# Performance work log

Measured on AMD Instinct MI355X. Metric: run time of the kernel, lower is better.

## Reference

```python
import jax, jax.numpy as jnp
import numpy as np
import math

B, S, D = 4, 2048, 1024
NUM_HEADS = 16
HEAD_DIM = D // NUM_HEADS


def setup_inputs() -> dict:
    key = jax.random.key(0)
    ks = jax.random.split(key, 6)
    scale = 1.0 / math.sqrt(D)
    batch = jax.random.normal(ks[0], (B, S, D), dtype=jnp.float32)
    w_query = jax.random.normal(ks[1], (D, D), dtype=jnp.float32) * scale
    w_key = jax.random.normal(ks[2], (D, D), dtype=jnp.float32) * scale
    w_value = jax.random.normal(ks[3], (D, D), dtype=jnp.float32) * scale
    out_w = jax.random.normal(ks[4], (D, D), dtype=jnp.float32) * scale
    out_b = jax.random.normal(ks[5], (D,), dtype=jnp.float32) * 0.01
    return {"batch": batch, "w_query": w_query, "w_key": w_key,
            "w_value": w_value, "out_w": out_w, "out_b": out_b}


def reference(batch, w_query, w_key, w_value, out_w, out_b):
    b, s, _ = batch.shape
    # QKV projections (Linear with no bias): x @ W^T, here weights stored as [D,D] applied as x@W
    q = (batch @ w_query).reshape(b, s, NUM_HEADS, HEAD_DIM)
    k = (batch @ w_key).reshape(b, s, NUM_HEADS, HEAD_DIM)
    v = (batch @ w_value).reshape(b, s, NUM_HEADS, HEAD_DIM)
    # scores: [b, h, s, s]
    scores = jnp.einsum('bqhd,bkhd->bhqk', q, k)
    causal = jnp.tril(jnp.ones((s, s), dtype=bool))
    scores = jnp.where(causal, scores, -jnp.inf)
    # original divides by sqrt(head_dim) AFTER masking (-inf stays -inf)
    weights = jax.nn.softmax(scores / math.sqrt(HEAD_DIM), axis=-1)
    # dropout_percent = 0 -> identity
    out = jnp.einsum('bhqk,bkhd->bqhd', weights, v).reshape(b, s, D)
    return out @ out_w + out_b
```

## Files before the change

kernel.cpp:

```cpp
#include <hip/hip_runtime.h>
#include <hip/hip_bf16.h>

#define S_LEN 2048
#define D_DIM 1024
#define NHEAD 16
#define HDIM  64
#define BATCH 4
#define MROWS (BATCH*S_LEN)
#define QKV_LD 3072

typedef short bf16x8 __attribute__((ext_vector_type(8)));
typedef float f32x4  __attribute__((ext_vector_type(4)));
typedef float f32x16 __attribute__((ext_vector_type(16)));
typedef unsigned short u16;

#if __has_builtin(__builtin_amdgcn_exp2f)
#define EXP2(x) __builtin_amdgcn_exp2f(x)
#else
#define EXP2(x) __expf((x) * 0.6931471805599453f)
#endif

__device__ inline u16 f2bf(float f) {
  union { float f; unsigned u; } v; v.f = f;
  unsigned r = v.u + 0x7fff + ((v.u >> 16) & 1);
  return (u16)(r >> 16);
}

__device__ inline unsigned cvtpk(float lo, float hi_) {
  unsigned d;
  asm("v_cvt_pk_bf16_f32 %0, %1, %2" : "=v"(d) : "v"(lo), "v"(hi_));
  return d;
}

__device__ inline void perm32swap(unsigned& a, unsigned& b) {
  asm volatile("v_permlane32_swap_b32 %0, %1" : "+v"(a), "+v"(b));
}

__device__ inline void gload_lds16(const void* g, void* l) {
  __builtin_amdgcn_global_load_lds(
      (const __attribute__((address_space(1))) void*)g,
      (__attribute__((address_space(3))) void*)l, 16, 0, 0);
}

__global__ void cvt_x_kernel(const float* __restrict__ x, u16* __restrict__ xb, int n4) {
  int i = blockIdx.x * 256 + threadIdx.x;
  if (i >= n4) return;
  float4 v = reinterpret_cast<const float4*>(x)[i];
  ushort4 o;
  o.x = f2bf(v.x); o.y = f2bf(v.y); o.z = f2bf(v.z); o.w = f2bf(v.w);
  reinterpret_cast<ushort4*>(xb)[i] = o;
}

__global__ void transpose_w_kernel(const float* __restrict__ w, u16* __restrict__ wt) {
  __shared__ float t[32][33];
  int tx = threadIdx.x, ty = threadIdx.y;
  int n0 = blockIdx.x * 32, k0 = blockIdx.y * 32;
#pragma unroll
  for (int j = 0; j < 32; j += 8)
    t[ty + j][tx] = w[(size_t)(k0 + ty + j) * D_DIM + n0 + tx];
  __syncthreads();
#pragma unroll
  for (int j = 0; j < 32; j += 8)
    wt[(size_t)(n0 + ty + j) * D_DIM + k0 + tx] = f2bf(t[tx][ty + j]);
}

__global__ __launch_bounds__(256) void pack_k_kernel(const u16* __restrict__ QKV,
                                                     u16* __restrict__ KP) {
  int tid = threadIdx.x;
  int j = blockIdx.x, bh = blockIdx.y;
  int s = tid >> 6, lane = tid & 63;
  int lq = lane & 31, hi = lane >> 5;
  int b = bh >> 4, h = bh & 15;
  const u16* src = QKV + (size_t)(b * S_LEN + j * 32 + lq) * QKV_LD
                   + 1024 + h * HDIM + s * 16 + hi * 8;
  bf16x8 v = *(const bf16x8*)src;
  *(bf16x8*)(KP + ((size_t)(bh * 64 + j) * 4 + s) * 512 + lane * 8) = v;
}

__global__ __launch_bounds__(256) void pack_v_kernel(const u16* __restrict__ QKV,
                                                     u16* __restrict__ VP) {
  int tid = threadIdx.x;
  int j = blockIdx.x, bh = blockIdx.y;
  int c = tid >> 6, lane = tid & 63;
  int lq = lane & 31, hi = lane >> 5;
  int b = bh >> 4, h = bh & 15;
  int d = (c >> 1) * 32 + lq;
  int s0 = j * 32 + (c & 1) * 16 + hi * 8;
  const u16* src = QKV + (size_t)(b * S_LEN + s0) * QKV_LD + 2048 + h * HDIM + d;
  u16 tmp[8];
#pragma unroll
  for (int e = 0; e < 8; ++e) tmp[e] = src[(size_t)e * QKV_LD];
  *(bf16x8*)(VP + ((size_t)(bh * 64 + j) * 4 + c) * 512 + lane * 8) = *(bf16x8*)tmp;
}

template <int EPI>
__global__ __launch_bounds__(256) void gemm_bt_kernel(
    const u16* __restrict__ A, const u16* __restrict__ Bt,
    void* __restrict__ Cv, const float* __restrict__ bias, int ldc) {
  __shared__ u16 lA[128 * 32];
  __shared__ u16 lB[128 * 32];
  const int tid = threadIdx.x, wid = tid >> 6, lane = tid & 63;
  const int bm = blockIdx.y, bn = blockIdx.x;
  const int fr = lane & 15, fq = lane >> 4;
  const int r0 = wid * 32;
  const int srow = lane >> 2, scol = (lane & 3) * 8;
  const u16* gA = A + (size_t)(bm * 128 + r0 + srow) * 1024 + scol;
  const u16* gB = Bt + (size_t)(bn * 128 + r0 + srow) * 1024 + scol;
  u16* lA0 = &lA[r0 * 32];
  u16* lB0 = &lB[r0 * 32];

  f32x4 acc[4][4] = {};
  const int wm = (wid >> 1) * 64, wn = (wid & 1) * 64;

  for (int k0 = 0; k0 < 1024; k0 += 32) {
    gload_lds16(gA + k0,             lA0);
    gload_lds16(gA + k0 + 16 * 1024, lA0 + 16 * 32);
    gload_lds16(gB + k0,             lB0);
    gload_lds16(gB + k0 + 16 * 1024, lB0 + 16 * 32);
    __syncthreads();
    bf16x8 fa[4], fb[4];
#pragma unroll
    for (int i = 0; i < 4; i++) {
      fa[i] = *(const bf16x8*)&lA[(wm + i * 16 + fr) * 32 + fq * 8];
      fb[i] = *(const bf16x8*)&lB[(wn + i * 16 + fr) * 32 + fq * 8];
    }
#pragma unroll
    for (int i = 0; i < 4; i++)
#pragma unroll
      for (int j = 0; j < 4; j++)
        acc[i][j] = __builtin_amdgcn_mfma_f32_16x16x32_bf16(fa[i], fb[j], acc[i][j], 0, 0, 0);
    __syncthreads();
  }

#pragma unroll
  for (int i = 0; i < 4; i++)
#pragma unroll
    for (int j = 0; j < 4; j++)
#pragma unroll
      for (int r = 0; r < 4; r++) {
        int row = bm * 128 + wm + i * 16 + fq * 4 + r;
        int col = bn * 128 + wn + j * 16 + fr;
        if (EPI == 0) {
          ((u16*)Cv)[(size_t)row * ldc + col] = f2bf(acc[i][j][r]);
        } else {
          ((float*)Cv)[(size_t)row * ldc + col] = acc[i][j][r] + bias[col];
        }
      }
}

__global__ __launch_bounds__(256) void attn_kernel(
    const u16* __restrict__ QKV, const u16* __restrict__ KP,
    const u16* __restrict__ VP, u16* __restrict__ O) {
  const int tid = threadIdx.x, wid = tid >> 6, lane = tid & 63;
  const int lq = lane & 31, hi = lane >> 5;
  int f = blockIdx.x;
  int xcd = f & 7, kk = f >> 3;
  int bh = xcd * 8 + (kk & 7);
  int qblk = 15 - (kk >> 3);
  int b = bh >> 4, h = bh & 15;
  int q0 = qblk * 128 + wid * 32;
  int q = q0 + lq;

  const u16* Qrow = QKV + (size_t)(b * S_LEN + q) * QKV_LD + h * HDIM;
  bf16x8 qf[4];
#pragma unroll
  for (int s = 0; s < 4; s++)
    qf[s] = *(const bf16x8*)(Qrow + s * 16 + hi * 8);

  const bf16x8* KPt = (const bf16x8*)KP + (size_t)bh * 64 * 4 * 64;
  const bf16x8* VPt = (const bf16x8*)VP + (size_t)bh * 64 * 4 * 64;

  f32x16 acc0 = {}, acc1 = {};
  float m = -3.0e38f, l = 0.f;
  const int nt = qblk * 4 + wid + 1;

  for (int t = 0; t < nt; ++t) {
    const int j0 = t * 32;
    const size_t fb = (size_t)t * 4 * 64 + lane;
    bf16x8 kf0 = KPt[fb], kf1 = KPt[fb + 64], kf2 = KPt[fb + 128], kf3 = KPt[fb + 192];
    bf16x8 vf00 = VPt[fb], vf01 = VPt[fb + 64], vf10 = VPt[fb + 128], vf11 = VPt[fb + 192];

    f32x16 sa = {};
    __builtin_amdgcn_s_setprio(1);
    sa = __builtin_amdgcn_mfma_f32_32x32x16_bf16(kf0, qf[0], sa, 0, 0, 0);
    sa = __builtin_amdgcn_mfma_f32_32x32x16_bf16(kf1, qf[1], sa, 0, 0, 0);
    sa = __builtin_amdgcn_mfma_f32_32x32x16_bf16(kf2, qf[2], sa, 0, 0, 0);
    sa = __builtin_amdgcn_mfma_f32_32x32x16_bf16(kf3, qf[3], sa, 0, 0, 0);
    __builtin_amdgcn_s_setprio(0);

    float p[16];
#pragma unroll
    for (int r = 0; r < 16; ++r) p[r] = sa[r] * 0.1803368801f;

    if (t == nt - 1) {
#pragma unroll
      for (int r = 0; r < 16; ++r) {
        int kidx = j0 + (r & 3) + 8 * (r >> 2) + 4 * hi;
        if (kidx > q) p[r] = -3.0e38f;
      }
    }

    float x8[8], x4[4], x2[2];
#pragma unroll
    for (int i = 0; i < 8; ++i) x8[i] = fmaxf(p[2 * i], p[2 * i + 1]);
#pragma unroll
    for (int i = 0; i < 4; ++i) x4[i] = fmaxf(x8[2 * i], x8[2 * i + 1]);
    x2[0] = fmaxf(x4[0], x4[1]); x2[1] = fmaxf(x4[2], x4[3]);
    float pm = fmaxf(x2[0], x2[1]);
    pm = fmaxf(pm, __shfl_xor(pm, 32));

    if (__any(pm > m + 11.5f)) {
      float mn = fmaxf(m, pm);
      float sc = EXP2(m - mn);
      l *= sc;
#pragma unroll
      for (int r = 0; r < 16; ++r) { acc0[r] *= sc; acc1[r] *= sc; }
      m = mn;
    }

    float rs = 0.f;
#pragma unroll
    for (int r = 0; r < 16; ++r) { p[r] = EXP2(p[r] - m); rs += p[r]; }
    rs += __shfl_xor(rs, 32);
    l += rs;

    unsigned c0 = cvtpk(p[0],  p[1]),  c1 = cvtpk(p[2],  p[3]);
    unsigned c2 = cvtpk(p[4],  p[5]),  c3 = cvtpk(p[6],  p[7]);
    unsigned c4 = cvtpk(p[8],  p[9]),  c5 = cvtpk(p[10], p[11]);
    unsigned c6 = cvtpk(p[12], p[13]), c7 = cvtpk(p[14], p[15]);
    perm32swap(c0, c2); perm32swap(c1, c3);
    perm32swap(c4, c6); perm32swap(c5, c7);
    union U4 { unsigned u[4]; bf16x8 v; } F0, F1;
    F0.u[0] = c0; F0.u[1] = c1; F0.u[2] = c2; F0.u[3] = c3;
    F1.u[0] = c4; F1.u[1] = c5; F1.u[2] = c6; F1.u[3] = c7;

    __builtin_amdgcn_s_setprio(1);
    acc0 = __builtin_amdgcn_mfma_f32_32x32x16_bf16(vf00, F0.v, acc0, 0, 0, 0);
    acc0 = __builtin_amdgcn_mfma_f32_32x32x16_bf16(vf01, F1.v, acc0, 0, 0, 0);
    acc1 = __builtin_amdgcn_mfma_f32_32x32x16_bf16(vf10, F0.v, acc1, 0, 0, 0);
    acc1 = __builtin_amdgcn_mfma_f32_32x32x16_bf16(vf11, F1.v, acc1, 0, 0, 0);
    __builtin_amdgcn_s_setprio(0);
  }

  float inv = 1.f / l;
  u16* Orow = O + (size_t)(b * S_LEN + q) * D_DIM + h * HDIM;
#pragma unroll
  for (int g = 0; g < 4; ++g) {
    ushort4 o4;
    o4.x = f2bf(acc0[g * 4 + 0] * inv);
    o4.y = f2bf(acc0[g * 4 + 1] * inv);
    o4.z = f2bf(acc0[g * 4 + 2] * inv);
    o4.w = f2bf(acc0[g * 4 + 3] * inv);
    *(ushort4*)(Orow + 8 * g + 4 * hi) = o4;
  }
#pragma unroll
  for (int g = 0; g < 4; ++g) {
    ushort4 o4;
    o4.x = f2bf(acc1[g * 4 + 0] * inv);
    o4.y = f2bf(acc1[g * 4 + 1] * inv);
    o4.z = f2bf(acc1[g * 4 + 2] * inv);
    o4.w = f2bf(acc1[g * 4 + 3] * inv);
    *(ushort4*)(Orow + 32 + 8 * g + 4 * hi) = o4;
  }
}

extern "C" void kernel_launch(void* const* d_in, const int* in_sizes, int n_in,
                              void* d_out, int out_size, void* d_ws, size_t ws_size,
                              hipStream_t stream) {
  const float* x  = (const float*)d_in[0];
  const float* wq = (const float*)d_in[1];
  const float* wk = (const float*)d_in[2];
  const float* wv = (const float*)d_in[3];
  const float* wo = (const float*)d_in[4];
  const float* ob = (const float*)d_in[5];
  float* out = (float*)d_out;

  char* ws = (char*)d_ws;
  u16* Xb    = (u16*)(ws);
  u16* Ab    = (u16*)(ws);
  u16* QKV   = (u16*)(ws + (size_t)16 * 1024 * 1024);
  u16* KPb   = (u16*)(ws + (size_t)64 * 1024 * 1024);
  u16* VPb   = (u16*)(ws + (size_t)80 * 1024 * 1024);
  u16* WqkvT = (u16*)(ws + (size_t)96 * 1024 * 1024);
  u16* WoT   = (u16*)(ws + (size_t)102 * 1024 * 1024);

  cvt_x_kernel<<<(MROWS * D_DIM / 4) / 256, 256, 0, stream>>>(x, Xb, MROWS * D_DIM / 4);

  dim3 tb(32, 8);
  transpose_w_kernel<<<dim3(32, 32), tb, 0, stream>>>(wq, WqkvT);
  transpose_w_kernel<<<dim3(32, 32), tb, 0, stream>>>(wk, WqkvT + 1024 * 1024);
  transpose_w_kernel<<<dim3(32, 32), tb, 0, stream>>>(wv, WqkvT + 2 * 1024 * 1024);
  transpose_w_kernel<<<dim3(32, 32), tb, 0, stream>>>(wo, WoT);

  gemm_bt_kernel<0><<<dim3(QKV_LD / 128, MROWS / 128), 256, 0, stream>>>(
      Xb, WqkvT, QKV, nullptr, QKV_LD);

  pack_k_kernel<<<dim3(64, 64), 256, 0, stream>>>(QKV, KPb);
  pack_v_kernel<<<dim3(64, 64), 256, 0, stream>>>(QKV, VPb);

  attn_kernel<<<dim3(1024), 256, 0, stream>>>(QKV, KPb, VPb, Ab);

  gemm_bt_kernel<1><<<dim3(D_DIM / 128, MROWS / 128), 256, 0, stream>>>(
      Ab, WoT, out, ob, D_DIM);
}
```

Measured before the change: 187.0 us.

## Replace GEMM with 256x256 eight-wave double-buffered ping-pong MFMA kernel

Both projection GEMMs move to a new kernel that uses 256x256 output tiles, 8 waves and K-steps of 64. Loads go directly from global memory into LDS, which is double-buffered with an XOR swizzle to avoid bank conflicts, and they are interleaved with MFMA quadrants using explicit barriers, vmcnt waits and setprio. An XCD-aware block swizzle is added for L2 locality. The goal is to hide global load latency and raise data reuse per tile, which the old single-buffered 128x128 kernel with 32-wide K could not do. In exchange the kernel uses far more registers and LDS, and the hand-scheduled waits are fragile.

```diff
diff --git a/kernel.cpp b/kernel.cpp
--- a/kernel.cpp
+++ b/kernel.cpp
@@ -93,57 +93,116 @@
   *(bf16x8*)(VP + ((size_t)(bh * 64 + j) * 4 + c) * 512 + lane * 8) = *(bf16x8*)tmp;
 }
 
+#define BAR() asm volatile("s_barrier" ::: "memory")
+#define WAITV(N) asm volatile("s_waitcnt vmcnt(" #N ")" ::: "memory")
+#define PRIO1() __builtin_amdgcn_s_setprio(1)
+#define PRIO0() __builtin_amdgcn_s_setprio(0)
+
+#define STAGE(bufv, ab, h, gptr) {                                              \
+  const u16* _s = (gptr) + (size_t)(wid * 8 + (lane >> 3)) * 1024               \
+                  + (size_t)((((lane & 7) ^ (lane >> 3)) * 8));                 \
+  gload_lds16(_s,              &lds[bufv][ab][(h) * 8192 + wid * 512]);         \
+  gload_lds16(_s + 64 * 1024,  &lds[bufv][ab][(h) * 8192 + 4096 + wid * 512]); }
+
+#define RDF(bufv, ab, r_, c2_) \
+  (*(const bf16x8*)((const char*)&lds[bufv][ab][0] + ((r_) * 128 + ((c2_) ^ rxA))))
+
+#define READ_ALO(bufv) { _Pragma("unroll") for (int mt = 0; mt < 4; mt++)       \
+  _Pragma("unroll") for (int ks = 0; ks < 2; ks++)                              \
+    fa[mt][ks] = RDF(bufv, 0, wm + mt * 16 + fr, ks * 64 + fq * 16); }
+#define READ_AHI(bufv) { _Pragma("unroll") for (int mt = 0; mt < 4; mt++)       \
+  _Pragma("unroll") for (int ks = 0; ks < 2; ks++)                              \
+    fa[4 + mt][ks] = RDF(bufv, 0, wm + 64 + mt * 16 + fr, ks * 64 + fq * 16); }
+#define READ_BLO(bufv) { _Pragma("unroll") for (int nt = 0; nt < 2; nt++)       \
+  _Pragma("unroll") for (int ks = 0; ks < 2; ks++)                              \
+    fb[nt][ks] = RDF(bufv, 1, wn + nt * 16 + fr, ks * 64 + fq * 16); }
+#define READ_BHI(bufv) { _Pragma("unroll") for (int nt = 0; nt < 2; nt++)       \
+  _Pragma("unroll") for (int ks = 0; ks < 2; ks++)                              \
+    fb[2 + nt][ks] = RDF(bufv, 1, wn + 32 + nt * 16 + fr, ks * 64 + fq * 16); }
+
+#define QUAD(mh, nh) { PRIO1();                                                 \
+  _Pragma("unroll") for (int mt = 0; mt < 4; mt++)                              \
+  _Pragma("unroll") for (int nt = 0; nt < 2; nt++)                              \
+  _Pragma("unroll") for (int ks = 0; ks < 2; ks++)                              \
+    acc[(mh) * 4 + mt][(nh) * 2 + nt] = __builtin_amdgcn_mfma_f32_16x16x32_bf16(\
+        fa[(mh) * 4 + mt][ks], fb[(nh) * 2 + nt][ks],                           \
+        acc[(mh) * 4 + mt][(nh) * 2 + nt], 0, 0, 0);                            \
+  PRIO0(); }
+
+#define APTR(h, kt) (A  + (size_t)(bm * 256 + (h) * 128) * 1024 + (size_t)(kt) * 64)
+#define BPTR(h, kt) (Bt + (size_t)(bn * 256 + (h) * 128) * 1024 + (size_t)(kt) * 64)
+
 template <int EPI>
-__global__ __launch_bounds__(256) void gemm_bt_kernel(
+__global__ __launch_bounds__(512, 2) void gemm8p_kernel(
     const u16* __restrict__ A, const u16* __restrict__ Bt,
-    void* __restrict__ Cv, const float* __restrict__ bias, int ldc) {
-  __shared__ u16 lA[128 * 32];
-  __shared__ u16 lB[128 * 32];
+    void* __restrict__ Cv, const float* __restrict__ bias, int nbx, int ldc) {
+  __shared__ u16 lds[2][2][16384];
   const int tid = threadIdx.x, wid = tid >> 6, lane = tid & 63;
-  const int bm = blockIdx.y, bn = blockIdx.x;
   const int fr = lane & 15, fq = lane >> 4;
-  const int r0 = wid * 32;
-  const int srow = lane >> 2, scol = (lane & 3) * 8;
-  const u16* gA = A + (size_t)(bm * 128 + r0 + srow) * 1024 + scol;
-  const u16* gB = Bt + (size_t)(bn * 128 + r0 + srow) * 1024 + scol;
-  u16* lA0 = &lA[r0 * 32];
-  u16* lB0 = &lB[r0 * 32];
-
-  f32x4 acc[4][4] = {};
-  const int wm = (wid >> 1) * 64, wn = (wid & 1) * 64;
-
-  for (int k0 = 0; k0 < 1024; k0 += 32) {
-    gload_lds16(gA + k0,             lA0);
-    gload_lds16(gA + k0 + 16 * 1024, lA0 + 16 * 32);
-    gload_lds16(gB + k0,             lB0);
-    gload_lds16(gB + k0 + 16 * 1024, lB0 + 16 * 32);
-    __syncthreads();
-    bf16x8 fa[4], fb[4];
-#pragma unroll
-    for (int i = 0; i < 4; i++) {
-      fa[i] = *(const bf16x8*)&lA[(wm + i * 16 + fr) * 32 + fq * 8];
-      fb[i] = *(const bf16x8*)&lB[(wn + i * 16 + fr) * 32 + fq * 8];
-    }
-#pragma unroll
-    for (int i = 0; i < 4; i++)
-#pragma unroll
-      for (int j = 0; j < 4; j++)
-        acc[i][j] = __builtin_amdgcn_mfma_f32_16x16x32_bf16(fa[i], fb[j], acc[i][j], 0, 0, 0);
-    __syncthreads();
+  const int wm = (wid >> 2) * 128, wn = (wid & 3) * 64;
+  const int rxA = (fr & 7) << 4;
+  const int nwg = gridDim.x, cpx = nwg >> 3, wg = blockIdx.x;
+  const int swz = (wg & 7) * cpx + (wg >> 3);
+  const int bm = swz / nbx, bn = swz % nbx;
+
+  bf16x8 fa[8][2], fb[4][2];
+  f32x4 acc[8][4] = {};
+
+  STAGE(0, 0, 0, APTR(0, 0)); STAGE(0, 0, 1, APTR(1, 0));
+  STAGE(0, 1, 0, BPTR(0, 0)); STAGE(0, 1, 1, BPTR(1, 0));
+  STAGE(1, 0, 0, APTR(0, 1)); STAGE(1, 0, 1, APTR(1, 1));
+  WAITV(4);
+  BAR();
+
+  for (int i = 0; i < 8; i++) {
+    const int t = 2 * i;
+    const int t2 = (t + 2 < 16) ? t + 2 : 0;
+    const int t3 = (t + 3 < 16) ? t + 3 : 0;
+    READ_ALO(0); READ_BLO(0);
+    STAGE(1, 1, 0, BPTR(0, t + 1));
+    BAR(); QUAD(0, 0); BAR();
+
+    READ_AHI(0);
+    STAGE(1, 1, 1, BPTR(1, t + 1));
+    BAR(); QUAD(1, 0); BAR();
+
+    READ_BHI(0);
+    STAGE(0, 0, 0, APTR(0, t2));
+    BAR(); QUAD(0, 1); BAR();
+
+    STAGE(0, 0, 1, APTR(1, t2));
+    WAITV(4);
+    BAR(); QUAD(1, 1); BAR();
+    READ_ALO(1); READ_BLO(1);
+    STAGE(0, 1, 0, BPTR(0, t2));
+    BAR(); QUAD(0, 0); BAR();
+
+    READ_AHI(1);
+    STAGE(0, 1, 1, BPTR(1, t2));
+    BAR(); QUAD(1, 0); BAR();
+
+    READ_BHI(1);
+    STAGE(1, 0, 0, APTR(0, t3));
+    BAR(); QUAD(0, 1); BAR();
+
+    STAGE(1, 0, 1, APTR(1, t3));
+    WAITV(4);
+    BAR(); QUAD(1, 1); BAR();
   }
-
-#pragma unroll
-  for (int i = 0; i < 4; i++)
-#pragma unroll
-    for (int j = 0; j < 4; j++)
-#pragma unroll
-      for (int r = 0; r < 4; r++) {
-        int row = bm * 128 + wm + i * 16 + fq * 4 + r;
-        int col = bn * 128 + wn + j * 16 + fr;
+  WAITV(0);
+
+#pragma unroll
+  for (int mt = 0; mt < 8; mt++)
+#pragma unroll
+    for (int nt = 0; nt < 4; nt++)
+#pragma unroll
+      for (int j = 0; j < 4; j++) {
+        int row = bm * 256 + wm + mt * 16 + fq * 4 + j;
+        int col = bn * 256 + wn + nt * 16 + fr;
         if (EPI == 0) {
-          ((u16*)Cv)[(size_t)row * ldc + col] = f2bf(acc[i][j][r]);
+          ((u16*)Cv)[(size_t)row * ldc + col] = f2bf(acc[mt][nt][j]);
         } else {
-          ((float*)Cv)[(size_t)row * ldc + col] = acc[i][j][r] + bias[col];
+          ((float*)Cv)[(size_t)row * ldc + col] = acc[mt][nt][j] + bias[col];
         }
       }
 }
@@ -292,14 +351,14 @@
   transpose_w_kernel<<<dim3(32, 32), tb, 0, stream>>>(wv, WqkvT + 2 * 1024 * 1024);
   transpose_w_kernel<<<dim3(32, 32), tb, 0, stream>>>(wo, WoT);
 
-  gemm_bt_kernel<0><<<dim3(QKV_LD / 128, MROWS / 128), 256, 0, stream>>>(
-      Xb, WqkvT, QKV, nullptr, QKV_LD);
+  gemm8p_kernel<0><<<dim3((MROWS / 256) * (QKV_LD / 256)), 512, 0, stream>>>(
+      Xb, WqkvT, QKV, nullptr, QKV_LD / 256, QKV_LD);
 
   pack_k_kernel<<<dim3(64, 64), 256, 0, stream>>>(QKV, KPb);
   pack_v_kernel<<<dim3(64, 64), 256, 0, stream>>>(QKV, VPb);
 
   attn_kernel<<<dim3(1024), 256, 0, stream>>>(QKV, KPb, VPb, Ab);
 
-  gemm_bt_kernel<1><<<dim3(D_DIM / 128, MROWS / 128), 256, 0, stream>>>(
-      Ab, WoT, out, ob, D_DIM);
-}
+  gemm8p_kernel<1><<<dim3((MROWS / 256) * (D_DIM / 256)), 512, 0, stream>>>(
+      Ab, WoT, out, ob, D_DIM / 256, D_DIM);
+}
```

Result: slower. 196.4 us (+5.0%).

## Fuse K/V packing into QKV GEMM epilogue and merge weight transposes

Applied to the files above, without the earlier changes.

The QKV projection GEMM now writes Q to a plain buffer and scatters K and V directly into the packed layouts the attention kernel consumes. This removes the separate pack_k and pack_v kernels and the round trip of K/V through a 3072-wide QKV buffer. The four weight-transpose launches are merged into one launch using blockIdx.z. The cost is a scattered, less coalesced store pattern in the GEMM epilogue, with 2-byte scalar stores for K.

```diff
diff --git a/kernel.cpp b/kernel.cpp
--- a/kernel.cpp
+++ b/kernel.cpp
@@ -7,7 +7,6 @@
 #define HDIM  64
 #define BATCH 4
 #define MROWS (BATCH*S_LEN)
-#define QKV_LD 3072
 
 typedef short bf16x8 __attribute__((ext_vector_type(8)));
 typedef float f32x4  __attribute__((ext_vector_type(4)));
@@ -51,8 +50,13 @@
   reinterpret_cast<ushort4*>(xb)[i] = o;
 }
 
-__global__ void transpose_w_kernel(const float* __restrict__ w, u16* __restrict__ wt) {
+__global__ void transpose_w4_kernel(const float* __restrict__ wq, const float* __restrict__ wk,
+                                    const float* __restrict__ wv, const float* __restrict__ wo,
+                                    u16* __restrict__ wqkvT, u16* __restrict__ woT) {
   __shared__ float t[32][33];
+  int z = blockIdx.z;
+  const float* w = (z == 0) ? wq : (z == 1) ? wk : (z == 2) ? wv : wo;
+  u16* wt = (z < 3) ? (wqkvT + (size_t)z * 1024 * 1024) : woT;
   int tx = threadIdx.x, ty = threadIdx.y;
   int n0 = blockIdx.x * 32, k0 = blockIdx.y * 32;
 #pragma unroll
@@ -64,39 +68,11 @@
     wt[(size_t)(n0 + ty + j) * D_DIM + k0 + tx] = f2bf(t[tx][ty + j]);
 }
 
-__global__ __launch_bounds__(256) void pack_k_kernel(const u16* __restrict__ QKV,
-                                                     u16* __restrict__ KP) {
-  int tid = threadIdx.x;
-  int j = blockIdx.x, bh = blockIdx.y;
-  int s = tid >> 6, lane = tid & 63;
-  int lq = lane & 31, hi = lane >> 5;
-  int b = bh >> 4, h = bh & 15;
-  const u16* src = QKV + (size_t)(b * S_LEN + j * 32 + lq) * QKV_LD
-                   + 1024 + h * HDIM + s * 16 + hi * 8;
-  bf16x8 v = *(const bf16x8*)src;
-  *(bf16x8*)(KP + ((size_t)(bh * 64 + j) * 4 + s) * 512 + lane * 8) = v;
-}
-
-__global__ __launch_bounds__(256) void pack_v_kernel(const u16* __restrict__ QKV,
-                                                     u16* __restrict__ VP) {
-  int tid = threadIdx.x;
-  int j = blockIdx.x, bh = blockIdx.y;
-  int c = tid >> 6, lane = tid & 63;
-  int lq = lane & 31, hi = lane >> 5;
-  int b = bh >> 4, h = bh & 15;
-  int d = (c >> 1) * 32 + lq;
-  int s0 = j * 32 + (c & 1) * 16 + hi * 8;
-  const u16* src = QKV + (size_t)(b * S_LEN + s0) * QKV_LD + 2048 + h * HDIM + d;
-  u16 tmp[8];
-#pragma unroll
-  for (int e = 0; e < 8; ++e) tmp[e] = src[(size_t)e * QKV_LD];
-  *(bf16x8*)(VP + ((size_t)(bh * 64 + j) * 4 + c) * 512 + lane * 8) = *(bf16x8*)tmp;
-}
-
 template <int EPI>
 __global__ __launch_bounds__(256) void gemm_bt_kernel(
     const u16* __restrict__ A, const u16* __restrict__ Bt,
-    void* __restrict__ Cv, const float* __restrict__ bias, int ldc) {
+    void* __restrict__ Cv, u16* __restrict__ KP, u16* __restrict__ VP,
+    const float* __restrict__ bias) {
   __shared__ u16 lA[128 * 32];
   __shared__ u16 lB[128 * 32];
   const int tid = threadIdx.x, wid = tid >> 6, lane = tid & 63;
@@ -132,24 +108,74 @@
     __syncthreads();
   }
 
-#pragma unroll
-  for (int i = 0; i < 4; i++)
-#pragma unroll
-    for (int j = 0; j < 4; j++)
-#pragma unroll
-      for (int r = 0; r < 4; r++) {
-        int row = bm * 128 + wm + i * 16 + fq * 4 + r;
-        int col = bn * 128 + wn + j * 16 + fr;
-        if (EPI == 0) {
-          ((u16*)Cv)[(size_t)row * ldc + col] = f2bf(acc[i][j][r]);
-        } else {
-          ((float*)Cv)[(size_t)row * ldc + col] = acc[i][j][r] + bias[col];
+  if (EPI == 1) {
+#pragma unroll
+    for (int i = 0; i < 4; i++)
+#pragma unroll
+      for (int j = 0; j < 4; j++)
+#pragma unroll
+        for (int r = 0; r < 4; r++) {
+          int row = bm * 128 + wm + i * 16 + fq * 4 + r;
+          int col = bn * 128 + wn + j * 16 + fr;
+          ((float*)Cv)[(size_t)row * 1024 + col] = acc[i][j][r] + bias[col];
+        }
+    return;
+  }
+
+  const int col0 = bn * 128;
+  if (col0 < 1024) {
+#pragma unroll
+    for (int i = 0; i < 4; i++)
+#pragma unroll
+      for (int j = 0; j < 4; j++)
+#pragma unroll
+        for (int r = 0; r < 4; r++) {
+          int row = bm * 128 + wm + i * 16 + fq * 4 + r;
+          int col = col0 + wn + j * 16 + fr;
+          ((u16*)Cv)[(size_t)row * 1024 + col] = f2bf(acc[i][j][r]);
+        }
+  } else if (col0 < 2048) {
+#pragma unroll
+    for (int i = 0; i < 4; i++)
+#pragma unroll
+      for (int j = 0; j < 4; j++) {
+        int col = col0 + wn + j * 16 + fr;
+        int ck = col - 1024;
+        int h = ck >> 6, d = ck & 63;
+        int sfr = d >> 4, e = d & 7, hb = (d >> 3) & 1;
+#pragma unroll
+        for (int r = 0; r < 4; r++) {
+          int row = bm * 128 + wm + i * 16 + fq * 4 + r;
+          int b = row >> 11, sp = row & 2047;
+          int bh = b * 16 + h, jt = sp >> 5;
+          int lanep = (sp & 31) + 32 * hb;
+          KP[((size_t)(bh * 64 + jt) * 4 + sfr) * 512 + lanep * 8 + e] = f2bf(acc[i][j][r]);
         }
       }
+  } else {
+#pragma unroll
+    for (int i = 0; i < 4; i++)
+#pragma unroll
+      for (int j = 0; j < 4; j++) {
+        int col = col0 + wn + j * 16 + fr;
+        int cv = col - 2048;
+        int h = cv >> 6, d = cv & 63;
+        int R0 = bm * 128 + wm + i * 16 + fq * 4;
+        int b = R0 >> 11, sp0 = R0 & 2047;
+        int bh = b * 16 + h, jt = sp0 >> 5;
+        int c = (d >> 5) * 2 + ((sp0 >> 4) & 1);
+        int lanep = (d & 31) + 32 * ((sp0 >> 3) & 1);
+        int e0 = sp0 & 7;
+        ushort4 ov;
+        ov.x = f2bf(acc[i][j][0]); ov.y = f2bf(acc[i][j][1]);
+        ov.z = f2bf(acc[i][j][2]); ov.w = f2bf(acc[i][j][3]);
+        *(ushort4*)(VP + ((size_t)(bh * 64 + jt) * 4 + c) * 512 + lanep * 8 + e0) = ov;
+      }
+  }
 }
 
 __global__ __launch_bounds__(256) void attn_kernel(
-    const u16* __restrict__ QKV, const u16* __restrict__ KP,
+    const u16* __restrict__ Q, const u16* __restrict__ KP,
     const u16* __restrict__ VP, u16* __restrict__ O) {
   const int tid = threadIdx.x, wid = tid >> 6, lane = tid & 63;
   const int lq = lane & 31, hi = lane >> 5;
@@ -161,7 +187,7 @@
   int q0 = qblk * 128 + wid * 32;
   int q = q0 + lq;
 
-  const u16* Qrow = QKV + (size_t)(b * S_LEN + q) * QKV_LD + h * HDIM;
+  const u16* Qrow = Q + (size_t)(b * S_LEN + q) * D_DIM + h * HDIM;
   bf16x8 qf[4];
 #pragma unroll
   for (int s = 0; s < 4; s++)
@@ -278,28 +304,22 @@
   char* ws = (char*)d_ws;
   u16* Xb    = (u16*)(ws);
   u16* Ab    = (u16*)(ws);
-  u16* QKV   = (u16*)(ws + (size_t)16 * 1024 * 1024);
-  u16* KPb   = (u16*)(ws + (size_t)64 * 1024 * 1024);
-  u16* VPb   = (u16*)(ws + (size_t)80 * 1024 * 1024);
-  u16* WqkvT = (u16*)(ws + (size_t)96 * 1024 * 1024);
-  u16* WoT   = (u16*)(ws + (size_t)102 * 1024 * 1024);
+  u16* Qb    = (u16*)(ws + (size_t)16 * 1024 * 1024);
+  u16* KPb   = (u16*)(ws + (size_t)32 * 1024 * 1024);
+  u16* VPb   = (u16*)(ws + (size_t)48 * 1024 * 1024);
+  u16* WqkvT = (u16*)(ws + (size_t)64 * 1024 * 1024);
+  u16* WoT   = (u16*)(ws + (size_t)70 * 1024 * 1024);
 
   cvt_x_kernel<<<(MROWS * D_DIM / 4) / 256, 256, 0, stream>>>(x, Xb, MROWS * D_DIM / 4);
 
-  dim3 tb(32, 8);
-  transpose_w_kernel<<<dim3(32, 32), tb, 0, stream>>>(wq, WqkvT);
-  transpose_w_kernel<<<dim3(32, 32), tb, 0, stream>>>(wk, WqkvT + 1024 * 1024);
-  transpose_w_kernel<<<dim3(32, 32), tb, 0, stream>>>(wv, WqkvT + 2 * 1024 * 1024);
-  transpose_w_kernel<<<dim3(32, 32), tb, 0, stream>>>(wo, WoT);
-
-  gemm_bt_kernel<0><<<dim3(QKV_LD / 128, MROWS / 128), 256, 0, stream>>>(
-      Xb, WqkvT, QKV, nullptr, QKV_LD);
-
-  pack_k_kernel<<<dim3(64, 64), 256, 0, stream>>>(QKV, KPb);
-  pack_v_kernel<<<dim3(64, 64), 256, 0, stream>>>(QKV, VPb);
-
-  attn_kernel<<<dim3(1024), 256, 0, stream>>>(QKV, KPb, VPb, Ab);
-
-  gemm_bt_kernel<1><<<dim3(D_DIM / 128, MROWS / 128), 256, 0, stream>>>(
-      Ab, WoT, out, ob, D_DIM);
-}
+  transpose_w4_kernel<<<dim3(32, 32, 4), dim3(32, 8), 0, stream>>>(
+      wq, wk, wv, wo, WqkvT, WoT);
+
+  gemm_bt_kernel<0><<<dim3(24, 64), 256, 0, stream>>>(
+      Xb, WqkvT, Qb, KPb, VPb, nullptr);
+
+  attn_kernel<<<dim3(1024), 256, 0, stream>>>(Qb, KPb, VPb, Ab);
+
+  gemm_bt_kernel<1><<<dim3(8, 64), 256, 0, stream>>>(
+      Ab, WoT, out, nullptr, nullptr, ob);
+}
```

After: 177.6 us. -5.0%, faster.
